# Optimization experiments

Measured on AMD Instinct MI355X. Metric: run time of the kernel, lower is better.

The kernel has to match this reference:

```python
import jax, jax.numpy as jnp
import numpy as np

B, C, H, W = 4, 16, 32, 32
I = 256    # input_embedding_dim
E = 256    # decoded_embed_dim
L = 4      # num_blocks
S = 4      # scaling_factor
NCH = 64   # num_channels (embedding rows)
HID = 4 * E


def setup_inputs() -> dict:
    key = jax.random.key(0)
    ks = jax.random.split(key, 10)
    f = lambda k, sh: jax.random.normal(k, sh, jnp.float32) * 0.02
    return dict(
        x=jax.random.normal(ks[0], (B, I, H, W), jnp.float32),
        indices=jax.random.randint(ks[1], (B, C), 0, NCH),
        hk_w=f(ks[2], (NCH, I * E)),          # Hyperkernel weight embedding table
        hk_b=f(ks[3], (NCH, E)),              # Hyperkernel bias embedding table
        dw_w=f(ks[4], (L, E, 1, 7, 7)),       # depthwise conv weights per block
        dw_b=jnp.zeros((L, E), jnp.float32),
        ln_g=jnp.ones((L, E), jnp.float32),
        ln_b=jnp.zeros((L, E), jnp.float32),
        fc1_w=f(ks[5], (L, HID, E)),
        fc1_b=jnp.zeros((L, HID), jnp.float32),
        grn_g=jnp.zeros((L, HID), jnp.float32),  # GRN gamma init zeros (as in torch)
        grn_b=jnp.zeros((L, HID), jnp.float32),
        fc2_w=f(ks[6], (L, E, HID)),
        fc2_b=jnp.zeros((L, E), jnp.float32),
        pred_w=f(ks[7], (S * S * 2, E)),      # 1x1 conv == linear over channels
        pred_b=jnp.zeros((S * S * 2,), jnp.float32),
    )


def _grn(x, g, b, eps=1e-6):
    # x: [N,H,W,D]; L2 norm over spatial dims per channel
    gx = jnp.sqrt(jnp.sum(x * x, axis=(1, 2), keepdims=True))  # [N,1,1,D]
    nx = gx / (jnp.mean(gx, axis=-1, keepdims=True) + eps)
    return g * (x * nx) + b + x


def _convnext_block(x, dw_w, dw_b, ln_g, ln_b, fc1_w, fc1_b, grn_g, grn_b, fc2_w, fc2_b):
    # x: [N,E,H,W]
    res = x
    x = jax.lax.conv_general_dilated(
        x, dw_w, window_strides=(1, 1), padding=[(3, 3), (3, 3)],
        dimension_numbers=('NCHW', 'OIHW', 'NCHW'), feature_group_count=E)
    x = x + dw_b[None, :, None, None]
    x = x.transpose(0, 2, 3, 1)  # NHWC
    mu = x.mean(-1, keepdims=True)
    var = jnp.mean((x - mu) ** 2, axis=-1, keepdims=True)
    x = (x - mu) / jnp.sqrt(var + 1e-5) * ln_g + ln_b
    x = jax.nn.gelu(x @ fc1_w.T + fc1_b, approximate=False)
    x = _grn(x, grn_g, grn_b)
    x = x @ fc2_w.T + fc2_b
    return x.transpose(0, 3, 1, 2) + res


def reference(x, indices, hk_w, hk_b, dw_w, dw_b, ln_g, ln_b, fc1_w, fc1_b,
              grn_g, grn_b, fc2_w, fc2_b, pred_w, pred_b):
    # Hyperkernel, decoder/linear path: gather per-channel weights, einsum route
    w = hk_w[indices].reshape(B, C, I, E)                       # [B,C,I,E]
    h = jnp.einsum('bihw,bcie->bcehw', x, w)                    # [B,C,E,H,W]
    h = h + hk_b[indices][..., None, None]
    h = h.reshape(B * C, E, H, W)
    for l in range(L):
        h = _convnext_block(h, dw_w[l], dw_b[l], ln_g[l], ln_b[l],
                            fc1_w[l], fc1_b[l], grn_g[l], grn_b[l],
                            fc2_w[l], fc2_b[l])
    # pred 1x1 conv -> pixel-shuffle style rearrange
    p = jnp.einsum('nehw,oe->nohw', h, pred_w) + pred_b[None, :, None, None]
    p = p.reshape(B, C, S, S, 2, H, W)
    p = p.transpose(0, 1, 5, 2, 6, 3, 4)  # bcxyohw -> bchxwyo
    return p.reshape(B, C, H * S, W * S, 2)
```

## Files before the change

### kernel.cpp

```cpp
#include <hip/hip_runtime.h>
#include <hip/hip_bf16.h>
#include <math.h>


typedef __attribute__((ext_vector_type(8))) __bf16 bf16x8;
typedef __attribute__((ext_vector_type(4))) float f32x4;

__device__ __forceinline__ short f2bf(float f) {
  unsigned u = __float_as_uint(f);
  unsigned r = (u + 0x7FFFu + ((u >> 16) & 1u)) >> 16;
  return (short)r;
}
__device__ __forceinline__ float bf2f(short s) {
  return __uint_as_float(((unsigned)(unsigned short)s) << 16);
}
__device__ __forceinline__ int pack2(short a, short b) {
  return (int)(unsigned short)a | ((int)(unsigned short)b << 16);
}
__device__ __forceinline__ float gelu(float x) {
  float t = __builtin_fmaf(0.0713548162f * x * x, x, 1.59576912f * x);
  return x / (1.f + __expf(-t));
}

__device__ __forceinline__ void gload16(const short* g, short* l) {
  __builtin_amdgcn_global_load_lds(
      (const __attribute__((address_space(1))) void*)(g),
      (__attribute__((address_space(3))) void*)(l), 16, 0, 0);
}

__device__ __forceinline__ float block_sum(float v, float* red) {
#pragma unroll
  for (int o = 32; o > 0; o >>= 1) v += __shfl_down(v, o);
  int lane = threadIdx.x & 63, w = threadIdx.x >> 6;
  int nw = blockDim.x >> 6;
  if (lane == 0) red[w] = v;
  __syncthreads();
  if (threadIdx.x == 0) {
    float s = 0.f;
    for (int i = 0; i < nw; ++i) s += red[i];
    red[0] = s;
  }
  __syncthreads();
  float s = red[0];
  __syncthreads();
  return s;
}

template <int K>
__device__ __forceinline__ void gemm_core(const short* __restrict__ A, const short* __restrict__ Bt,
                                          int m0, int n0, short* As, short* Bs, f32x4 acc[4][4]) {
  const int tid = threadIdx.x;
  const int lane = tid & 63, wave = tid >> 6;
  const int wr = wave >> 1, wc = wave & 1;
  const int lr = lane & 15, kg = lane >> 4;
#pragma unroll
  for (int mi = 0; mi < 4; ++mi)
#pragma unroll
    for (int ni = 0; ni < 4; ++ni) acc[mi][ni] = f32x4{0.f, 0.f, 0.f, 0.f};
  const int sr = lane >> 2, sc = (lane & 3) * 8;
  const int ra0 = wave * 16, ra1 = wave * 16 + 64;
  const short* Ab = A + (size_t)m0 * K;
  const short* Bb = Bt + (size_t)n0 * K;
  for (int k0 = 0; k0 < K; k0 += 32) {
    gload16(Ab + (size_t)(ra0 + sr) * K + k0 + sc, As + ra0 * 32);
    gload16(Ab + (size_t)(ra1 + sr) * K + k0 + sc, As + ra1 * 32);
    gload16(Bb + (size_t)(ra0 + sr) * K + k0 + sc, Bs + ra0 * 32);
    gload16(Bb + (size_t)(ra1 + sr) * K + k0 + sc, Bs + ra1 * 32);
    __syncthreads();
    bf16x8 af[4], bfr[4];
#pragma unroll
    for (int mi = 0; mi < 4; ++mi) af[mi] = *(const bf16x8*)&As[(wr * 64 + mi * 16 + lr) * 32 + kg * 8];
#pragma unroll
    for (int ni = 0; ni < 4; ++ni) bfr[ni] = *(const bf16x8*)&Bs[(wc * 64 + ni * 16 + lr) * 32 + kg * 8];
#pragma unroll
    for (int mi = 0; mi < 4; ++mi)
#pragma unroll
      for (int ni = 0; ni < 4; ++ni)
        acc[mi][ni] = __builtin_amdgcn_mfma_f32_16x16x32_bf16(af[mi], bfr[ni], acc[mi][ni], 0, 0, 0);
    __syncthreads();
  }
}

template <int K>
__device__ __forceinline__ void gemm_core_n64(const short* __restrict__ A, const short* __restrict__ Bt,
                                              int m0, int n0, short* As, short* Bs, f32x4 acc[4][2]) {
  const int tid = threadIdx.x;
  const int lane = tid & 63, wave = tid >> 6;
  const int wr = wave >> 1, wc = wave & 1;
  const int lr = lane & 15, kg = lane >> 4;
#pragma unroll
  for (int mi = 0; mi < 4; ++mi)
#pragma unroll
    for (int ni = 0; ni < 2; ++ni) acc[mi][ni] = f32x4{0.f, 0.f, 0.f, 0.f};
  const int sr = lane >> 2, sc = (lane & 3) * 8;
  const int ra0 = wave * 16, ra1 = wave * 16 + 64;
  const short* Ab = A + (size_t)m0 * K;
  const short* Bb = Bt + (size_t)n0 * K;
  for (int k0 = 0; k0 < K; k0 += 32) {
    gload16(Ab + (size_t)(ra0 + sr) * K + k0 + sc, As + ra0 * 32);
    gload16(Ab + (size_t)(ra1 + sr) * K + k0 + sc, As + ra1 * 32);
    gload16(Bb + (size_t)(ra0 + sr) * K + k0 + sc, Bs + ra0 * 32);
    __syncthreads();
    bf16x8 af[4], bfr[2];
#pragma unroll
    for (int mi = 0; mi < 4; ++mi) af[mi] = *(const bf16x8*)&As[(wr * 64 + mi * 16 + lr) * 32 + kg * 8];
#pragma unroll
    for (int ni = 0; ni < 2; ++ni) bfr[ni] = *(const bf16x8*)&Bs[(wc * 32 + ni * 16 + lr) * 32 + kg * 8];
#pragma unroll
    for (int mi = 0; mi < 4; ++mi)
#pragma unroll
      for (int ni = 0; ni < 2; ++ni)
        acc[mi][ni] = __builtin_amdgcn_mfma_f32_16x16x32_bf16(af[mi], bfr[ni], acc[mi][ni], 0, 0, 0);
    __syncthreads();
  }
}

__global__ void k_cvt_w(const float* __restrict__ fc1w, const float* __restrict__ fc2w,
                        short* __restrict__ w1b, short* __restrict__ w2b) {
  int i = blockIdx.x * 256 + threadIdx.x;
  w1b[i] = f2bf(fc1w[i]);
  w2b[i] = f2bf(fc2w[i]);
}

__global__ void k_prep_xt(const float* __restrict__ x, short* __restrict__ xTb) {
  __shared__ float tile[32][33];
  int tx = threadIdx.x & 31, ty = threadIdx.x >> 5;
  int p0 = blockIdx.x * 32, i0 = blockIdx.y * 32, b = blockIdx.z;
#pragma unroll
  for (int r = 0; r < 4; ++r) {
    int i = ty + r * 8;
    tile[i][tx] = x[((size_t)b * 256 + i0 + i) * 1024 + p0 + tx];
  }
  __syncthreads();
#pragma unroll
  for (int r = 0; r < 4; ++r) {
    int p = ty + r * 8;
    xTb[((size_t)b * 1024 + p0 + p) * 256 + i0 + tx] = f2bf(tile[tx][p]);
  }
}

__global__ void k_prep_wt(const float* __restrict__ hkw, const int* __restrict__ idx,
                          short* __restrict__ Wt) {
  __shared__ float tile[32][33];
  int tx = threadIdx.x & 31, ty = threadIdx.x >> 5;
  int e0 = blockIdx.x * 32, i0 = blockIdx.y * 32, n = blockIdx.z;
  int ch = idx[n];
#pragma unroll
  for (int r = 0; r < 4; ++r) {
    int i = ty + r * 8;
    tile[i][tx] = hkw[(size_t)ch * 65536 + (size_t)(i0 + i) * 256 + e0 + tx];
  }
  __syncthreads();
#pragma unroll
  for (int r = 0; r < 4; ++r) {
    int e = ty + r * 8;
    Wt[((size_t)n * 256 + e0 + e) * 256 + i0 + tx] = f2bf(tile[tx][e]);
  }
}

__global__ void k_prep_misc(const float* __restrict__ grng, const float* __restrict__ grnb,
                            const float* __restrict__ fc2w, int* __restrict__ flag,
                            float* __restrict__ cvec) {
  __shared__ float red[8];
  int l = blockIdx.y;
  if (blockIdx.x == 0) {
    float any = 0.f;
    for (int d = threadIdx.x; d < 1024; d += 256)
      any += (grng[l * 1024 + d] != 0.f) ? 1.f : 0.f;
    float tot = block_sum(any, red);
    if (threadIdx.x == 0) flag[l] = (tot > 0.f) ? 1 : 0;
  } else {
    int e = blockIdx.x - 1;
    float s = 0.f;
    for (int d = threadIdx.x; d < 1024; d += 256)
      s += fc2w[((size_t)(l * 256 + e) << 10) + d] * grnb[l * 1024 + d];
    float tot = block_sum(s, red);
    if (threadIdx.x == 0) cvec[l * 256 + e] = tot;
  }
}

__global__ void __launch_bounds__(256) k_hypm(const short* __restrict__ Wt, const short* __restrict__ xTb,
                                              const int* __restrict__ idx, const float* __restrict__ hkb,
                                              short* __restrict__ hb) {
  __shared__ short As[4096], Bs[4096];
  f32x4 acc[4][4];
  int n = blockIdx.z;
  int m0 = blockIdx.y * 128, n0 = blockIdx.x * 128;
  gemm_core<256>(Wt + (size_t)n * 65536, xTb + (size_t)(n >> 4) * 262144, m0, n0, As, Bs, acc);
  int ch = idx[n];
  const int lane = threadIdx.x & 63, wave = threadIdx.x >> 6;
  const int wr = wave >> 1, wc = wave & 1, lr = lane & 15, kg = lane >> 4;
#pragma unroll
  for (int mi = 0; mi < 4; ++mi) {
    int ebase = m0 + wr * 64 + mi * 16 + kg * 4;
#pragma unroll
    for (int ni = 0; ni < 4; ++ni) {
      int p = n0 + wc * 64 + ni * 16 + lr;
      f32x4 v = acc[mi][ni];
#pragma unroll
      for (int r = 0; r < 4; ++r)
        hb[((size_t)(n * 256 + ebase + r) << 10) + p] = f2bf(v[r] + hkb[ch * 256 + ebase + r]);
    }
  }
}

__global__ void __launch_bounds__(256) k_conv(const short* __restrict__ hb, const float* __restrict__ dww,
                                              const float* __restrict__ dwb, short* __restrict__ tc, int l) {
  __shared__ float sm[38][40];
  int e = blockIdx.x, n = blockIdx.y;
  const short* plane = hb + (((size_t)(n * 256 + e)) << 10);
  const float* wv = dww + ((size_t)(l * 256 + e)) * 49;
  float w[49];
#pragma unroll
  for (int i = 0; i < 49; ++i) w[i] = wv[i];
  int tid = threadIdx.x;
  for (int i = tid; i < 38 * 40; i += 256) ((float*)sm)[i] = 0.f;
  __syncthreads();
  {
    const int* plane32 = (const int*)plane;
    for (int i = tid; i < 512; i += 256) {
      int v = plane32[i];
      int p = i * 2;
      int iy = p >> 5, ix = p & 31;
      sm[iy + 3][ix + 3] = bf2f((short)(v & 0xffff));
      sm[iy + 3][ix + 4] = bf2f((short)(v >> 16));
    }
  }
  __syncthreads();
  int x = tid & 31, y0 = (tid >> 5) * 4;
  float bias = dwb[l * 256 + e];
  float acc0 = bias, acc1 = bias, acc2 = bias, acc3 = bias;
#pragma unroll
  for (int r = 0; r < 10; ++r) {
#pragma unroll
    for (int c = 0; c < 7; ++c) {
      float v = sm[y0 + r][x + c];
      if (r <= 6)           acc0 += v * w[r * 7 + c];
      if (r >= 1 && r <= 7) acc1 += v * w[(r - 1) * 7 + c];
      if (r >= 2 && r <= 8) acc2 += v * w[(r - 2) * 7 + c];
      if (r >= 3)           acc3 += v * w[(r - 3) * 7 + c];
    }
  }
  short* outp = tc + (((size_t)(n * 256 + e)) << 10) + y0 * 32 + x;
  outp[0]  = f2bf(acc0);
  outp[32] = f2bf(acc1);
  outp[64] = f2bf(acc2);
  outp[96] = f2bf(acc3);
}

__global__ void __launch_bounds__(256) k_ln(const short* __restrict__ tc, const float* __restrict__ lng,
                                            const float* __restrict__ lnb, short* __restrict__ tb,
                                            float* __restrict__ gx, const int* __restrict__ flag, int l) {
  __shared__ float smT[32][261];
  __shared__ float muS[32], rsS[32];
  int n = blockIdx.y, p0 = blockIdx.x * 32;
  int tid = threadIdx.x;
  if (blockIdx.x == 0 && flag[l] != 0) {
#pragma unroll
    for (int r = 0; r < 4; ++r) gx[n * 1024 + r * 256 + tid] = 0.f;
  }
  const short* base = tc + ((size_t)n << 18) + p0;
  for (int i = tid; i < 8192; i += 256) {
    int e = i >> 5, p = i & 31;
    smT[p][e] = bf2f(base[(e << 10) + p]);
  }
  __syncthreads();
  {
    int j = tid & 7, p = tid >> 3;
    float s = 0.f, q = 0.f;
#pragma unroll
    for (int i = 0; i < 32; ++i) {
      float v = smT[p][j + i * 8];
      s += v; q += v * v;
    }
    s += __shfl_xor(s, 1); q += __shfl_xor(q, 1);
    s += __shfl_xor(s, 2); q += __shfl_xor(q, 2);
    s += __shfl_xor(s, 4); q += __shfl_xor(q, 4);
    if (j == 0) {
      float mu = s * (1.f / 256.f);
      float var = q * (1.f / 256.f) - mu * mu;
      muS[p] = mu;
      rsS[p] = rsqrtf(fmaxf(var, 0.f) + 1e-5f);
    }
  }
  __syncthreads();
  for (int i = tid; i < 8192; i += 256) {
    int p = i >> 8, e = i & 255;
    float v = (smT[p][e] - muS[p]) * rsS[p] * lng[l * 256 + e] + lnb[l * 256 + e];
    tb[((size_t)(n * 1024 + p0 + p)) * 256 + e] = f2bf(v);
  }
}

__global__ void __launch_bounds__(256) k_gx1(const short* __restrict__ w1b, const short* __restrict__ tb,
                                             const float* __restrict__ fc1b, float* __restrict__ gx,
                                             const int* __restrict__ flag, int l) {
  if (flag[l] == 0) return;
  __shared__ short As[4096], Bs[4096];
  f32x4 acc[4][4];
  int m0 = blockIdx.y * 128, n0 = blockIdx.x * 128;
  gemm_core<256>(w1b + (size_t)l * 262144, tb, m0, n0, As, Bs, acc);
  const int lane = threadIdx.x & 63, wave = threadIdx.x >> 6;
  const int wr = wave >> 1, kg = lane >> 4;
  int n = (n0 >> 10);
#pragma unroll
  for (int mi = 0; mi < 4; ++mi) {
    int dbase = m0 + wr * 64 + mi * 16 + kg * 4;
#pragma unroll
    for (int ni = 0; ni < 4; ++ni) {
      f32x4 v = acc[mi][ni];
#pragma unroll
      for (int r = 0; r < 4; ++r) {
        float g = gelu(v[r] + fc1b[l * 1024 + dbase + r]);
        atomicAdd(&gx[n * 1024 + dbase + r], g * g);
      }
    }
  }
}

__global__ void k_nx(const float* __restrict__ gx, float* __restrict__ nx,
                     const int* __restrict__ flag, int l) {
  int n = blockIdx.x, tid = threadIdx.x;
  if (flag[l] == 0) {
    for (int d = tid; d < 1024; d += 256) nx[n * 1024 + d] = 0.f;
    return;
  }
  __shared__ float red[8];
  __shared__ float sv[1024];
  float s = 0.f;
  for (int d = tid; d < 1024; d += 256) {
    float v = sqrtf(gx[n * 1024 + d]);
    sv[d] = v; s += v;
  }
  float tot = block_sum(s, red);
  float mean = tot * (1.f / 1024.f);
  for (int d = tid; d < 1024; d += 256) nx[n * 1024 + d] = sv[d] / (mean + 1e-6f);
}

__global__ void __launch_bounds__(256) k_fc1(const short* __restrict__ w1b, const short* __restrict__ tb,
                                             const float* __restrict__ fc1b, const float* __restrict__ grng,
                                             const float* __restrict__ nx, short* __restrict__ u,
                                             int l, int cbase) {
  __shared__ short As[4096], Bs[4096];
  f32x4 acc[4][4];
  int bid = blockIdx.x;
  int xcd = bid & 7, loc = bid >> 3;
  int nt = (xcd << 5) + (loc >> 3);
  int mt = loc & 7;
  int m0 = mt * 128, n0 = nt * 128;
  gemm_core<256>(w1b + (size_t)l * 262144, tb + (size_t)cbase * 256, m0, n0, As, Bs, acc);
  const int lane = threadIdx.x & 63, wave = threadIdx.x >> 6;
  const int wr = wave >> 1, wc = wave & 1, lr = lane & 15, kg = lane >> 4;
  int nimg = (cbase + n0) >> 10;
#pragma unroll
  for (int mi = 0; mi < 4; ++mi) {
    int dbase = m0 + wr * 64 + mi * 16 + kg * 4;
    float b0 = fc1b[l * 1024 + dbase + 0], b1 = fc1b[l * 1024 + dbase + 1];
    float b2 = fc1b[l * 1024 + dbase + 2], b3 = fc1b[l * 1024 + dbase + 3];
    float a0 = 1.f + grng[l * 1024 + dbase + 0] * nx[nimg * 1024 + dbase + 0];
    float a1 = 1.f + grng[l * 1024 + dbase + 1] * nx[nimg * 1024 + dbase + 1];
    float a2 = 1.f + grng[l * 1024 + dbase + 2] * nx[nimg * 1024 + dbase + 2];
    float a3 = 1.f + grng[l * 1024 + dbase + 3] * nx[nimg * 1024 + dbase + 3];
#pragma unroll
    for (int ni = 0; ni < 4; ++ni) {
      int pl = n0 + wc * 64 + ni * 16 + lr;
      f32x4 v = acc[mi][ni];
      short4 sv;
      sv.x = f2bf(gelu(v[0] + b0) * a0);
      sv.y = f2bf(gelu(v[1] + b1) * a1);
      sv.z = f2bf(gelu(v[2] + b2) * a2);
      sv.w = f2bf(gelu(v[3] + b3) * a3);
      *(short4*)&u[(size_t)pl * 1024 + dbase] = sv;
    }
  }
}

template <int LAST>
__global__ void __launch_bounds__(256) k_fc2(const short* __restrict__ w2b, const short* __restrict__ u,
                                             const float* __restrict__ fc2b, const float* __restrict__ cvec,
                                             short* __restrict__ hb, short* __restrict__ ht,
                                             int l, int cbase) {
  __shared__ short As[4096], Bs[2048];
  f32x4 acc[4][2];
  int bid = blockIdx.x;
  int xcd = bid & 7, loc = bid >> 3;
  int nt = (xcd << 6) + (loc >> 1);
  int mt = loc & 1;
  int m0 = mt * 128, n0 = nt * 64;
  gemm_core_n64<1024>(w2b + (size_t)l * 262144, u, m0, n0, As, Bs, acc);
  const int lane = threadIdx.x & 63, wave = threadIdx.x >> 6;
  const int wr = wave >> 1, wc = wave & 1, lr = lane & 15, kg = lane >> 4;
#pragma unroll
  for (int mi = 0; mi < 4; ++mi) {
    int ebase = m0 + wr * 64 + mi * 16 + kg * 4;
    float add0 = fc2b[l * 256 + ebase + 0] + cvec[l * 256 + ebase + 0];
    float add1 = fc2b[l * 256 + ebase + 1] + cvec[l * 256 + ebase + 1];
    float add2 = fc2b[l * 256 + ebase + 2] + cvec[l * 256 + ebase + 2];
    float add3 = fc2b[l * 256 + ebase + 3] + cvec[l * 256 + ebase + 3];
#pragma unroll
    for (int ni = 0; ni < 2; ++ni) {
      int P = cbase + n0 + wc * 32 + ni * 16 + lr;
      int n = P >> 10, p = P & 1023;
      f32x4 v = acc[mi][ni];
      short* hp0 = &hb[((size_t)(n * 256 + ebase) << 10) + p];
      float r0 = v[0] + add0 + bf2f(hp0[0]);
      float r1 = v[1] + add1 + bf2f(hp0[1 << 10]);
      float r2 = v[2] + add2 + bf2f(hp0[2 << 10]);
      float r3 = v[3] + add3 + bf2f(hp0[3 << 10]);
      if (LAST) {
        short* hr = &ht[(size_t)P * 256 + ebase];
        hr[0] = f2bf(r0); hr[1] = f2bf(r1); hr[2] = f2bf(r2); hr[3] = f2bf(r3);
      } else {
        hp0[0] = f2bf(r0); hp0[1 << 10] = f2bf(r1); hp0[2 << 10] = f2bf(r2); hp0[3 << 10] = f2bf(r3);
      }
    }
  }
}

__global__ void __launch_bounds__(128) k_pred2(const short* __restrict__ ht, const float* __restrict__ pw,
                                               const float* __restrict__ pb, float* __restrict__ out) {
  __shared__ short Aw[32 * 264];
  __shared__ short Bl[256 * 32];
  int tid = threadIdx.x;
  int n0 = blockIdx.x * 256;
  for (int i = tid; i < 8192; i += 128) {
    int o = i >> 8, e = i & 255;
    Aw[o * 264 + e] = f2bf(pw[i]);
  }
  const int lane = tid & 63, wave = tid >> 6;
  const int lr = lane & 15, kg = lane >> 4;
  const int sr = lane >> 2, sc = (lane & 3) * 8;
  f32x4 acc[2][8];
#pragma unroll
  for (int mi = 0; mi < 2; ++mi)
#pragma unroll
    for (int ni = 0; ni < 8; ++ni) acc[mi][ni] = f32x4{0.f, 0.f, 0.f, 0.f};
  __syncthreads();
  for (int k0 = 0; k0 < 256; k0 += 32) {
#pragma unroll
    for (int j = 0; j < 8; ++j) {
      int rb = wave * 128 + j * 16;
      gload16(ht + (size_t)(n0 + rb + sr) * 256 + k0 + sc, Bl + rb * 32);
    }
    __syncthreads();
    bf16x8 af[2], bfr[8];
#pragma unroll
    for (int mi = 0; mi < 2; ++mi) af[mi] = *(const bf16x8*)&Aw[(mi * 16 + lr) * 264 + k0 + kg * 8];
#pragma unroll
    for (int ni = 0; ni < 8; ++ni) bfr[ni] = *(const bf16x8*)&Bl[(wave * 128 + ni * 16 + lr) * 32 + kg * 8];
#pragma unroll
    for (int mi = 0; mi < 2; ++mi)
#pragma unroll
      for (int ni = 0; ni < 8; ++ni)
        acc[mi][ni] = __builtin_amdgcn_mfma_f32_16x16x32_bf16(af[mi], bfr[ni], acc[mi][ni], 0, 0, 0);
    __syncthreads();
  }
#pragma unroll
  for (int mi = 0; mi < 2; ++mi) {
#pragma unroll
    for (int ni = 0; ni < 8; ++ni) {
      int P = n0 + wave * 128 + ni * 16 + lr;
      int n = P >> 10, p = P & 1023;
      int y = p >> 5, xx = p & 31;
      f32x4 v = acc[mi][ni];
#pragma unroll
      for (int r = 0; r < 4; ++r) {
        int o = mi * 16 + kg * 4 + r;
        int s1 = o >> 3, s2 = (o >> 1) & 3, tt = o & 1;
        size_t oi = (((size_t)n * 128 + y * 4 + s1) * 128 + xx * 4 + s2) * 2 + tt;
        out[oi] = v[r] + pb[o];
      }
    }
  }
}

extern "C" void kernel_launch(void* const* d_in, const int* in_sizes, int n_in,
                              void* d_out, int out_size, void* d_ws, size_t ws_size,
                              hipStream_t stream) {
  const float* x    = (const float*)d_in[0];
  const int*   idx  = (const int*)d_in[1];
  const float* hkw  = (const float*)d_in[2];
  const float* hkb  = (const float*)d_in[3];
  const float* dww  = (const float*)d_in[4];
  const float* dwb  = (const float*)d_in[5];
  const float* lng  = (const float*)d_in[6];
  const float* lnb  = (const float*)d_in[7];
  const float* fc1w = (const float*)d_in[8];
  const float* fc1b = (const float*)d_in[9];
  const float* grng = (const float*)d_in[10];
  const float* grnb = (const float*)d_in[11];
  const float* fc2w = (const float*)d_in[12];
  const float* fc2b = (const float*)d_in[13];
  const float* pw   = (const float*)d_in[14];
  const float* pb   = (const float*)d_in[15];
  float* out = (float*)d_out;

  char* ws = (char*)d_ws;
  short* hb   = (short*)(ws);
  short* tb   = (short*)(ws + (32ull << 20));
  short* u    = (short*)(ws + (64ull << 20));
  short* tc   = (short*)(ws + (64ull << 20));
  short* Wt   = (short*)(ws + (64ull << 20));
  short* xTb  = (short*)(ws + (72ull << 20));
  short* w1b  = (short*)(ws + (128ull << 20));
  short* w2b  = (short*)(ws + (130ull << 20));
  float* gx   = (float*)(ws + (132ull << 20));
  float* nx   = (float*)(ws + (132ull << 20) + (1 << 18));
  float* cvec = (float*)(ws + (132ull << 20) + (2 << 18));
  int*   flag = (int*)  (ws + (132ull << 20) + (2 << 18) + 4096);

  k_cvt_w<<<4096, 256, 0, stream>>>(fc1w, fc2w, w1b, w2b);
  k_prep_misc<<<dim3(257, 4), 256, 0, stream>>>(grng, grnb, fc2w, flag, cvec);
  k_prep_xt<<<dim3(32, 8, 4), 256, 0, stream>>>(x, xTb);
  k_prep_wt<<<dim3(8, 8, 64), 256, 0, stream>>>(hkw, idx, Wt);
  k_hypm<<<dim3(8, 2, 64), 256, 0, stream>>>(Wt, xTb, idx, hkb, hb);
  for (int l = 0; l < 4; ++l) {
    k_conv<<<dim3(256, 64), 256, 0, stream>>>(hb, dww, dwb, tc, l);
    k_ln<<<dim3(32, 64), 256, 0, stream>>>(tc, lng, lnb, tb, gx, flag, l);
    k_gx1<<<dim3(512, 8), 256, 0, stream>>>(w1b, tb, fc1b, gx, flag, l);
    k_nx<<<64, 256, 0, stream>>>(gx, nx, flag, l);
    for (int c = 0; c < 2; ++c) {
      int cbase = c * 32768;
      k_fc1<<<2048, 256, 0, stream>>>(w1b, tb, fc1b, grng, nx, u, l, cbase);
      if (l < 3)
        k_fc2<0><<<1024, 256, 0, stream>>>(w2b, u, fc2b, cvec, hb, tb, l, cbase);
      else
        k_fc2<1><<<1024, 256, 0, stream>>>(w2b, u, fc2b, cvec, hb, tb, l, cbase);
    }
  }
  k_pred2<<<256, 128, 0, stream>>>(tb, pw, pb, out);
}
```

Before: 881.2 us.

## Fuse fc1 and fc2 GEMMs into one MLP kernel keeping hidden activations in LDS

Replaces the separate fc1 and fc2 kernels, which were launched in two chunks and round-tripped the 1024-wide hidden activation through global memory, with one kernel per 64-pixel tile. Each block stages its input rows in swizzled LDS, computes fc1 in 128-channel slices with GELU and GRN scaling, and feeds each slice straight into an fc2 accumulator held in registers. This removes the large intermediate write and read and halves the launch count. In exchange, each block uses about 64 KB of LDS and many accumulator registers, which lowers occupancy, and the weights are re-read from global or L2 by every block.

```diff
diff --git a/kernel.cpp b/kernel.cpp
--- a/kernel.cpp
+++ b/kernel.cpp
@@ -76,40 +76,6 @@
     for (int mi = 0; mi < 4; ++mi)
 #pragma unroll
       for (int ni = 0; ni < 4; ++ni)
-        acc[mi][ni] = __builtin_amdgcn_mfma_f32_16x16x32_bf16(af[mi], bfr[ni], acc[mi][ni], 0, 0, 0);
-    __syncthreads();
-  }
-}
-
-template <int K>
-__device__ __forceinline__ void gemm_core_n64(const short* __restrict__ A, const short* __restrict__ Bt,
-                                              int m0, int n0, short* As, short* Bs, f32x4 acc[4][2]) {
-  const int tid = threadIdx.x;
-  const int lane = tid & 63, wave = tid >> 6;
-  const int wr = wave >> 1, wc = wave & 1;
-  const int lr = lane & 15, kg = lane >> 4;
-#pragma unroll
-  for (int mi = 0; mi < 4; ++mi)
-#pragma unroll
-    for (int ni = 0; ni < 2; ++ni) acc[mi][ni] = f32x4{0.f, 0.f, 0.f, 0.f};
-  const int sr = lane >> 2, sc = (lane & 3) * 8;
-  const int ra0 = wave * 16, ra1 = wave * 16 + 64;
-  const short* Ab = A + (size_t)m0 * K;
-  const short* Bb = Bt + (size_t)n0 * K;
-  for (int k0 = 0; k0 < K; k0 += 32) {
-    gload16(Ab + (size_t)(ra0 + sr) * K + k0 + sc, As + ra0 * 32);
-    gload16(Ab + (size_t)(ra1 + sr) * K + k0 + sc, As + ra1 * 32);
-    gload16(Bb + (size_t)(ra0 + sr) * K + k0 + sc, Bs + ra0 * 32);
-    __syncthreads();
-    bf16x8 af[4], bfr[2];
-#pragma unroll
-    for (int mi = 0; mi < 4; ++mi) af[mi] = *(const bf16x8*)&As[(wr * 64 + mi * 16 + lr) * 32 + kg * 8];
-#pragma unroll
-    for (int ni = 0; ni < 2; ++ni) bfr[ni] = *(const bf16x8*)&Bs[(wc * 32 + ni * 16 + lr) * 32 + kg * 8];
-#pragma unroll
-    for (int mi = 0; mi < 4; ++mi)
-#pragma unroll
-      for (int ni = 0; ni < 2; ++ni)
         acc[mi][ni] = __builtin_amdgcn_mfma_f32_16x16x32_bf16(af[mi], bfr[ni], acc[mi][ni], 0, 0, 0);
     __syncthreads();
   }
@@ -336,81 +302,136 @@
   for (int d = tid; d < 1024; d += 256) nx[n * 1024 + d] = sv[d] / (mean + 1e-6f);
 }
 
-__global__ void __launch_bounds__(256) k_fc1(const short* __restrict__ w1b, const short* __restrict__ tb,
-                                             const float* __restrict__ fc1b, const float* __restrict__ grng,
-                                             const float* __restrict__ nx, short* __restrict__ u,
-                                             int l, int cbase) {
-  __shared__ short As[4096], Bs[4096];
-  f32x4 acc[4][4];
+template <int LAST>
+__global__ void __launch_bounds__(256) k_mlpf(const short* __restrict__ w1b, const short* __restrict__ w2b,
+                                              const short* tb,
+                                              const float* __restrict__ fc1b, const float* __restrict__ grng,
+                                              const float* __restrict__ nx,
+                                              const float* __restrict__ fc2b, const float* __restrict__ cvec,
+                                              short* __restrict__ hb, short* ht, int l) {
+  __shared__ short Tb[64 * 256];
+  __shared__ short Ws[8192];
+  __shared__ short uL[64 * 128];
+  const int tid = threadIdx.x;
+  const int lane = tid & 63, wave = tid >> 6;
+  const int wr = wave >> 1, wc = wave & 1;
+  const int lr = lane & 15, kg = lane >> 4;
+  const int sr = lane >> 2, sc = (lane & 3) * 8;
   int bid = blockIdx.x;
-  int xcd = bid & 7, loc = bid >> 3;
-  int nt = (xcd << 5) + (loc >> 3);
-  int mt = loc & 7;
-  int m0 = mt * 128, n0 = nt * 128;
-  gemm_core<256>(w1b + (size_t)l * 262144, tb + (size_t)cbase * 256, m0, n0, As, Bs, acc);
-  const int lane = threadIdx.x & 63, wave = threadIdx.x >> 6;
-  const int wr = wave >> 1, wc = wave & 1, lr = lane & 15, kg = lane >> 4;
-  int nimg = (cbase + n0) >> 10;
-#pragma unroll
-  for (int mi = 0; mi < 4; ++mi) {
-    int dbase = m0 + wr * 64 + mi * 16 + kg * 4;
-    float b0 = fc1b[l * 1024 + dbase + 0], b1 = fc1b[l * 1024 + dbase + 1];
-    float b2 = fc1b[l * 1024 + dbase + 2], b3 = fc1b[l * 1024 + dbase + 3];
-    float a0 = 1.f + grng[l * 1024 + dbase + 0] * nx[nimg * 1024 + dbase + 0];
-    float a1 = 1.f + grng[l * 1024 + dbase + 1] * nx[nimg * 1024 + dbase + 1];
-    float a2 = 1.f + grng[l * 1024 + dbase + 2] * nx[nimg * 1024 + dbase + 2];
-    float a3 = 1.f + grng[l * 1024 + dbase + 3] * nx[nimg * 1024 + dbase + 3];
-#pragma unroll
-    for (int ni = 0; ni < 4; ++ni) {
-      int pl = n0 + wc * 64 + ni * 16 + lr;
-      f32x4 v = acc[mi][ni];
-      short4 sv;
-      sv.x = f2bf(gelu(v[0] + b0) * a0);
-      sv.y = f2bf(gelu(v[1] + b1) * a1);
-      sv.z = f2bf(gelu(v[2] + b2) * a2);
-      sv.w = f2bf(gelu(v[3] + b3) * a3);
-      *(short4*)&u[(size_t)pl * 1024 + dbase] = sv;
-    }
-  }
-}
-
-template <int LAST>
-__global__ void __launch_bounds__(256) k_fc2(const short* __restrict__ w2b, const short* __restrict__ u,
-                                             const float* __restrict__ fc2b, const float* __restrict__ cvec,
-                                             short* __restrict__ hb, short* __restrict__ ht,
-                                             int l, int cbase) {
-  __shared__ short As[4096], Bs[2048];
-  f32x4 acc[4][2];
-  int bid = blockIdx.x;
-  int xcd = bid & 7, loc = bid >> 3;
-  int nt = (xcd << 6) + (loc >> 1);
-  int mt = loc & 1;
-  int m0 = mt * 128, n0 = nt * 64;
-  gemm_core_n64<1024>(w2b + (size_t)l * 262144, u, m0, n0, As, Bs, acc);
-  const int lane = threadIdx.x & 63, wave = threadIdx.x >> 6;
-  const int wr = wave >> 1, wc = wave & 1, lr = lane & 15, kg = lane >> 4;
-#pragma unroll
-  for (int mi = 0; mi < 4; ++mi) {
-    int ebase = m0 + wr * 64 + mi * 16 + kg * 4;
-    float add0 = fc2b[l * 256 + ebase + 0] + cvec[l * 256 + ebase + 0];
-    float add1 = fc2b[l * 256 + ebase + 1] + cvec[l * 256 + ebase + 1];
-    float add2 = fc2b[l * 256 + ebase + 2] + cvec[l * 256 + ebase + 2];
-    float add3 = fc2b[l * 256 + ebase + 3] + cvec[l * 256 + ebase + 3];
+  int tile = (bid & 7) * 128 + (bid >> 3);
+  int px0 = tile * 64;
+  int nimg = px0 >> 10;
+  const short* w1p = w1b + (size_t)l * 262144;
+  const short* w2p = w2b + (size_t)l * 262144;
+
+#pragma unroll
+  for (int j = 0; j < 8; ++j) {
+    int id = j * 256 + tid;
+    int px = id >> 5, c = (id & 31) * 8;
+    int4 v = *(const int4*)&tb[((size_t)(px0 + px)) * 256 + c];
+    *(int4*)&Tb[px * 256 + (c ^ ((px & 7) << 3))] = v;
+  }
+  f32x4 acc2[8][2];
+#pragma unroll
+  for (int mi = 0; mi < 8; ++mi)
+#pragma unroll
+    for (int ni = 0; ni < 2; ++ni) acc2[mi][ni] = f32x4{0.f, 0.f, 0.f, 0.f};
+  __syncthreads();
+
+  for (int dc = 0; dc < 8; ++dc) {
+    f32x4 acc1[4][2];
+#pragma unroll
+    for (int mi = 0; mi < 4; ++mi)
+#pragma unroll
+      for (int ni = 0; ni < 2; ++ni) acc1[mi][ni] = f32x4{0.f, 0.f, 0.f, 0.f};
+    for (int k0 = 0; k0 < 256; k0 += 32) {
+      gload16(w1p + (size_t)(dc * 128 + wave * 16 + sr) * 256 + k0 + sc, Ws + (wave * 16) * 32);
+      gload16(w1p + (size_t)(dc * 128 + wave * 16 + 64 + sr) * 256 + k0 + sc, Ws + (wave * 16 + 64) * 32);
+      __syncthreads();
+      bf16x8 af[4], bfr[2];
+#pragma unroll
+      for (int mi = 0; mi < 4; ++mi) af[mi] = *(const bf16x8*)&Ws[(wr * 64 + mi * 16 + lr) * 32 + kg * 8];
+#pragma unroll
+      for (int ni = 0; ni < 2; ++ni) {
+        int px = wc * 32 + ni * 16 + lr;
+        bfr[ni] = *(const bf16x8*)&Tb[px * 256 + ((k0 + kg * 8) ^ ((px & 7) << 3))];
+      }
+#pragma unroll
+      for (int mi = 0; mi < 4; ++mi)
+#pragma unroll
+        for (int ni = 0; ni < 2; ++ni)
+          acc1[mi][ni] = __builtin_amdgcn_mfma_f32_16x16x32_bf16(af[mi], bfr[ni], acc1[mi][ni], 0, 0, 0);
+      __syncthreads();
+    }
+#pragma unroll
+    for (int mi = 0; mi < 4; ++mi) {
+      int d0 = dc * 128 + wr * 64 + mi * 16 + kg * 4;
+      float b0 = fc1b[l * 1024 + d0 + 0], b1 = fc1b[l * 1024 + d0 + 1];
+      float b2 = fc1b[l * 1024 + d0 + 2], b3 = fc1b[l * 1024 + d0 + 3];
+      float a0 = 1.f + grng[l * 1024 + d0 + 0] * nx[nimg * 1024 + d0 + 0];
+      float a1 = 1.f + grng[l * 1024 + d0 + 1] * nx[nimg * 1024 + d0 + 1];
+      float a2 = 1.f + grng[l * 1024 + d0 + 2] * nx[nimg * 1024 + d0 + 2];
+      float a3 = 1.f + grng[l * 1024 + d0 + 3] * nx[nimg * 1024 + d0 + 3];
+      int dloc = wr * 64 + mi * 16 + kg * 4;
+#pragma unroll
+      for (int ni = 0; ni < 2; ++ni) {
+        int px = wc * 32 + ni * 16 + lr;
+        f32x4 v = acc1[mi][ni];
+        short4 sv;
+        sv.x = f2bf(gelu(v[0] + b0) * a0);
+        sv.y = f2bf(gelu(v[1] + b1) * a1);
+        sv.z = f2bf(gelu(v[2] + b2) * a2);
+        sv.w = f2bf(gelu(v[3] + b3) * a3);
+        *(short4*)&uL[px * 128 + (dloc ^ ((px & 7) << 3))] = sv;
+      }
+    }
+    __syncthreads();
+    for (int k0 = 0; k0 < 128; k0 += 32) {
+#pragma unroll
+      for (int j = 0; j < 4; ++j)
+        gload16(w2p + (size_t)(wave * 16 + j * 64 + sr) * 1024 + dc * 128 + k0 + sc,
+                Ws + (wave * 16 + j * 64) * 32);
+      __syncthreads();
+      bf16x8 af8[8], bfr[2];
+#pragma unroll
+      for (int mi = 0; mi < 8; ++mi) af8[mi] = *(const bf16x8*)&Ws[(wr * 128 + mi * 16 + lr) * 32 + kg * 8];
+#pragma unroll
+      for (int ni = 0; ni < 2; ++ni) {
+        int px = wc * 32 + ni * 16 + lr;
+        bfr[ni] = *(const bf16x8*)&uL[px * 128 + ((k0 + kg * 8) ^ ((px & 7) << 3))];
+      }
+#pragma unroll
+      for (int mi = 0; mi < 8; ++mi)
+#pragma unroll
+        for (int ni = 0; ni < 2; ++ni)
+          acc2[mi][ni] = __builtin_amdgcn_mfma_f32_16x16x32_bf16(af8[mi], bfr[ni], acc2[mi][ni], 0, 0, 0);
+      __syncthreads();
+    }
+  }
+#pragma unroll
+  for (int mi = 0; mi < 8; ++mi) {
+    int e = wr * 128 + mi * 16 + kg * 4;
+    float add0 = fc2b[l * 256 + e + 0] + cvec[l * 256 + e + 0];
+    float add1 = fc2b[l * 256 + e + 1] + cvec[l * 256 + e + 1];
+    float add2 = fc2b[l * 256 + e + 2] + cvec[l * 256 + e + 2];
+    float add3 = fc2b[l * 256 + e + 3] + cvec[l * 256 + e + 3];
 #pragma unroll
     for (int ni = 0; ni < 2; ++ni) {
-      int P = cbase + n0 + wc * 32 + ni * 16 + lr;
-      int n = P >> 10, p = P & 1023;
-      f32x4 v = acc[mi][ni];
-      short* hp0 = &hb[((size_t)(n * 256 + ebase) << 10) + p];
-      float r0 = v[0] + add0 + bf2f(hp0[0]);
-      float r1 = v[1] + add1 + bf2f(hp0[1 << 10]);
-      float r2 = v[2] + add2 + bf2f(hp0[2 << 10]);
-      float r3 = v[3] + add3 + bf2f(hp0[3 << 10]);
+      int pxl = wc * 32 + ni * 16 + lr;
+      int P = px0 + pxl;
+      int p = P & 1023;
+      f32x4 v = acc2[mi][ni];
+      short* hp = &hb[((size_t)(nimg * 256 + e) << 10) + p];
+      float r0 = v[0] + add0 + bf2f(hp[0]);
+      float r1 = v[1] + add1 + bf2f(hp[1 << 10]);
+      float r2 = v[2] + add2 + bf2f(hp[2 << 10]);
+      float r3 = v[3] + add3 + bf2f(hp[3 << 10]);
       if (LAST) {
-        short* hr = &ht[(size_t)P * 256 + ebase];
-        hr[0] = f2bf(r0); hr[1] = f2bf(r1); hr[2] = f2bf(r2); hr[3] = f2bf(r3);
+        short4 sv;
+        sv.x = f2bf(r0); sv.y = f2bf(r1); sv.z = f2bf(r2); sv.w = f2bf(r3);
+        *(short4*)&ht[(size_t)P * 256 + e] = sv;
       } else {
-        hp0[0] = f2bf(r0); hp0[1 << 10] = f2bf(r1); hp0[2 << 10] = f2bf(r2); hp0[3 << 10] = f2bf(r3);
+        hp[0] = f2bf(r0); hp[1 << 10] = f2bf(r1); hp[2 << 10] = f2bf(r2); hp[3 << 10] = f2bf(r3);
       }
     }
   }
@@ -497,7 +518,6 @@
   char* ws = (char*)d_ws;
   short* hb   = (short*)(ws);
   short* tb   = (short*)(ws + (32ull << 20));
-  short* u    = (short*)(ws + (64ull << 20));
   short* tc   = (short*)(ws + (64ull << 20));
   short* Wt   = (short*)(ws + (64ull << 20));
   short* xTb  = (short*)(ws + (72ull << 20));
@@ -518,14 +538,10 @@
     k_ln<<<dim3(32, 64), 256, 0, stream>>>(tc, lng, lnb, tb, gx, flag, l);
     k_gx1<<<dim3(512, 8), 256, 0, stream>>>(w1b, tb, fc1b, gx, flag, l);
     k_nx<<<64, 256, 0, stream>>>(gx, nx, flag, l);
-    for (int c = 0; c < 2; ++c) {
-      int cbase = c * 32768;
-      k_fc1<<<2048, 256, 0, stream>>>(w1b, tb, fc1b, grng, nx, u, l, cbase);
-      if (l < 3)
-        k_fc2<0><<<1024, 256, 0, stream>>>(w2b, u, fc2b, cvec, hb, tb, l, cbase);
-      else
-        k_fc2<1><<<1024, 256, 0, stream>>>(w2b, u, fc2b, cvec, hb, tb, l, cbase);
-    }
+    if (l < 3)
+      k_mlpf<0><<<1024, 256, 0, stream>>>(w1b, w2b, tb, fc1b, grng, nx, fc2b, cvec, hb, tb, l);
+    else
+      k_mlpf<1><<<1024, 256, 0, stream>>>(w1b, w2b, tb, fc1b, grng, nx, fc2b, cvec, hb, tb, l);
   }
   k_pred2<<<256, 128, 0, stream>>>(tb, pw, pb, out);
 }
```

Measured after the change: 900.1 us. 1.02x slower.

## Use K=64 tiles with XOR-swizzled LDS layout for fc1 GEMMs

Applied to the files above, without the earlier changes.

Adds a GEMM core that stages 64-wide K slices per iteration instead of 32, halving the number of barrier pairs per tile. The fc1 weights and the layernorm output are pre-permuted in global memory with an XOR swizzle on 8-element groups keyed by row, so the direct-to-LDS loads land in a bank-conflict-free layout for the MFMA fragment reads. This doubles LDS use per block, which may lower occupancy, and couples the producer kernels' storage layout to this consumer.

```diff
diff --git a/kernel.cpp b/kernel.cpp
--- a/kernel.cpp
+++ b/kernel.cpp
@@ -82,6 +82,54 @@
 }
 
 template <int K>
+__device__ __forceinline__ void gemm_core_k64(const short* __restrict__ A, const short* __restrict__ Bt,
+                                              int m0, int n0, short* As, short* Bs, f32x4 acc[4][4]) {
+  const int tid = threadIdx.x;
+  const int lane = tid & 63, wave = tid >> 6;
+  const int wr = wave >> 1, wc = wave & 1;
+  const int lr = lane & 15, kg = lane >> 4;
+#pragma unroll
+  for (int mi = 0; mi < 4; ++mi)
+#pragma unroll
+    for (int ni = 0; ni < 4; ++ni) acc[mi][ni] = f32x4{0.f, 0.f, 0.f, 0.f};
+  const int sr = lane >> 3;
+  const int sc = (lane & 7) * 8;
+  const short* Ab = A + (size_t)m0 * K;
+  const short* Bb = Bt + (size_t)n0 * K;
+  for (int k0 = 0; k0 < K; k0 += 64) {
+#pragma unroll
+    for (int j = 0; j < 4; ++j) {
+      int r = wave * 8 + j * 32;
+      gload16(Ab + (size_t)(r + sr) * K + k0 + sc, As + r * 64);
+      gload16(Bb + (size_t)(r + sr) * K + k0 + sc, Bs + r * 64);
+    }
+    __syncthreads();
+#pragma unroll
+    for (int ks = 0; ks < 2; ++ks) {
+      bf16x8 af[4], bfr[4];
+#pragma unroll
+      for (int mi = 0; mi < 4; ++mi) {
+        int R = wr * 64 + mi * 16 + lr;
+        int s = ks * 4 + kg;
+        af[mi] = *(const bf16x8*)&As[R * 64 + ((s ^ (R & 7)) << 3)];
+      }
+#pragma unroll
+      for (int ni = 0; ni < 4; ++ni) {
+        int R = wc * 64 + ni * 16 + lr;
+        int s = ks * 4 + kg;
+        bfr[ni] = *(const bf16x8*)&Bs[R * 64 + ((s ^ (R & 7)) << 3)];
+      }
+#pragma unroll
+      for (int mi = 0; mi < 4; ++mi)
+#pragma unroll
+        for (int ni = 0; ni < 4; ++ni)
+          acc[mi][ni] = __builtin_amdgcn_mfma_f32_16x16x32_bf16(af[mi], bfr[ni], acc[mi][ni], 0, 0, 0);
+    }
+    __syncthreads();
+  }
+}
+
+template <int K>
 __device__ __forceinline__ void gemm_core_n64(const short* __restrict__ A, const short* __restrict__ Bt,
                                               int m0, int n0, short* As, short* Bs, f32x4 acc[4][2]) {
   const int tid = threadIdx.x;
@@ -118,7 +166,10 @@
 __global__ void k_cvt_w(const float* __restrict__ fc1w, const float* __restrict__ fc2w,
                         short* __restrict__ w1b, short* __restrict__ w2b) {
   int i = blockIdx.x * 256 + threadIdx.x;
-  w1b[i] = f2bf(fc1w[i]);
+  int d7 = (i >> 8) & 7;
+  int e = i & 255;
+  int es = (e & 0xC0) | (((((e >> 3) & 7) ^ d7)) << 3) | (e & 7);
+  w1b[(i & ~255) | es] = f2bf(fc1w[i]);
   w2b[i] = f2bf(fc2w[i]);
 }
 
@@ -286,8 +337,10 @@
   __syncthreads();
   for (int i = tid; i < 8192; i += 256) {
     int p = i >> 8, e = i & 255;
+    int px = n * 1024 + p0 + p;
     float v = (smT[p][e] - muS[p]) * rsS[p] * lng[l * 256 + e] + lnb[l * 256 + e];
-    tb[((size_t)(n * 1024 + p0 + p)) * 256 + e] = f2bf(v);
+    int es = (e & 0xC0) | ((((e >> 3) & 7) ^ (px & 7)) << 3) | (e & 7);
+    tb[((size_t)px) * 256 + es] = f2bf(v);
   }
 }
 
@@ -295,10 +348,10 @@
                                              const float* __restrict__ fc1b, float* __restrict__ gx,
                                              const int* __restrict__ flag, int l) {
   if (flag[l] == 0) return;
-  __shared__ short As[4096], Bs[4096];
+  __shared__ short As[8192], Bs[8192];
   f32x4 acc[4][4];
   int m0 = blockIdx.y * 128, n0 = blockIdx.x * 128;
-  gemm_core<256>(w1b + (size_t)l * 262144, tb, m0, n0, As, Bs, acc);
+  gemm_core_k64<256>(w1b + (size_t)l * 262144, tb, m0, n0, As, Bs, acc);
   const int lane = threadIdx.x & 63, wave = threadIdx.x >> 6;
   const int wr = wave >> 1, kg = lane >> 4;
   int n = (n0 >> 10);
@@ -340,14 +393,14 @@
                                              const float* __restrict__ fc1b, const float* __restrict__ grng,
                                              const float* __restrict__ nx, short* __restrict__ u,
                                              int l, int cbase) {
-  __shared__ short As[4096], Bs[4096];
+  __shared__ short As[8192], Bs[8192];
   f32x4 acc[4][4];
   int bid = blockIdx.x;
   int xcd = bid & 7, loc = bid >> 3;
   int nt = (xcd << 5) + (loc >> 3);
   int mt = loc & 7;
   int m0 = mt * 128, n0 = nt * 128;
-  gemm_core<256>(w1b + (size_t)l * 262144, tb + (size_t)cbase * 256, m0, n0, As, Bs, acc);
+  gemm_core_k64<256>(w1b + (size_t)l * 262144, tb + (size_t)cbase * 256, m0, n0, As, Bs, acc);
   const int lane = threadIdx.x & 63, wave = threadIdx.x >> 6;
   const int wr = wave >> 1, wc = wave & 1, lr = lane & 15, kg = lane >> 4;
   int nimg = (cbase + n0) >> 10;
```

Result: faster. 849.7 us (-3.6%).
